# Optimization experiments

Measured on AMD Instinct MI355X. Metric: run time of the kernel, lower is better.

Reference implementation:

```python
import jax, jax.numpy as jnp
import numpy as np


def setup_inputs() -> dict:
    key = jax.random.key(0)
    ks = jax.random.split(key, 6)
    H = 1024
    NB = 5
    B = H  # required by the module's gate broadcasting (gate shape [B] * candidate [B,H])
    T = 128
    return {
        "features": jax.random.normal(ks[0], (B, T, H), dtype=jnp.float32),
        "states": jax.random.normal(ks[1], (NB * H,), dtype=jnp.float32),
        "Uw": jax.random.normal(ks[2], (H, H), dtype=jnp.float32) * 0.02,
        "Vw": jax.random.normal(ks[3], (H, H), dtype=jnp.float32) * 0.02,
        "Ww": jax.random.normal(ks[4], (H, H), dtype=jnp.float32) * 0.02,
        "keys": jax.random.normal(ks[5], (NB, H), dtype=jnp.float32) * 0.02,
        "prelu_a": jnp.ones((H,), dtype=jnp.float32),
    }


def reference(features, states, Uw, Vw, Ww, keys, prelu_a):
    # features: [B, T, H]; take CLS token (input_all_tokens=True)
    enc = features[:, 0, :]                      # [B, H]
    NB, H = keys.shape
    h = states.reshape(NB, H)                    # chunked states, [NB, H]

    # gate_i = sigmoid(enc @ h_i + enc @ key_i), vectorized over blocks -> [B, NB]
    gate = jax.nn.sigmoid(enc @ (h + keys).T)

    # candidate_i = PReLU(U(h_i) + V(key_i) + W(enc)) -> [NB, B, H]
    pre = (h @ Uw.T + keys @ Vw.T)[:, None, :] + (enc @ Ww.T)[None, :, :]
    cand = jnp.where(pre >= 0, pre, prelu_a * pre)

    # torch broadcasting of gate [B] against [B, H] aligns trailing dims (B == H),
    # so gate indexes the FEATURE axis: new[i, b, j] = h[i, j] + gate[j, i] * cand[i, b, j]
    new = h[:, None, :] + gate.T[:, None, :] * cand  # [NB, B, H]

    # in-place zero replacement aliases hidden_i in the original, so zeros -> 0.1 -> 1 after normalize
    new = jnp.where(new == 0, jnp.asarray(0.1, new.dtype), new)
    new = new / jnp.abs(new)

    # torch.cat(new_states) along dim 0 -> [NB*B, H]
    return new.reshape(NB * new.shape[1], H)
```

## Files before the change

kernel.cpp:

```cpp
#include <hip/hip_runtime.h>

#define H 1024
#define NB 5
#define TSTRIDE 131072

#define BM 64
#define BN 64
#define BK 32
#define LDA 68

__device__ __forceinline__ float sign_val(float h, float g, float pre, float a) {
    float cand = (pre >= 0.0f) ? pre : a * pre;
    float v = h + g * cand;
    if (v == 0.0f) v = 0.1f;
    return (v > 0.0f) ? 1.0f : -1.0f;
}

__global__ __launch_bounds__(256) void prep_kernel(
    const float* __restrict__ features,
    const float* __restrict__ states,
    const float* __restrict__ Uw,
    const float* __restrict__ Vw,
    const float* __restrict__ keys,
    float* __restrict__ gateT,
    float* __restrict__ baseT)
{
    const int j = blockIdx.x;
    const int tid = threadIdx.x;
    float accg[NB] = {0.f, 0.f, 0.f, 0.f, 0.f};
    float accb[NB] = {0.f, 0.f, 0.f, 0.f, 0.f};
    const float* encRow = features + (size_t)j * TSTRIDE;
    const float* uRow = Uw + (size_t)j * H;
    const float* vRow = Vw + (size_t)j * H;
    for (int k = tid; k < H; k += 256) {
        const float e = encRow[k];
        const float u = uRow[k];
        const float v = vRow[k];
        #pragma unroll
        for (int n = 0; n < NB; ++n) {
            const float hk = states[n * H + k];
            const float ky = keys[n * H + k];
            accg[n] += e * (hk + ky);
            accb[n] += hk * u + ky * v;
        }
    }
    __shared__ float red[2 * NB][4];
    #pragma unroll
    for (int n = 0; n < NB; ++n) {
        float g = accg[n], b = accb[n];
        #pragma unroll
        for (int off = 32; off > 0; off >>= 1) {
            g += __shfl_down(g, (unsigned)off, 64);
            b += __shfl_down(b, (unsigned)off, 64);
        }
        if ((tid & 63) == 0) {
            red[n][tid >> 6] = g;
            red[NB + n][tid >> 6] = b;
        }
    }
    __syncthreads();
    if (tid < 2 * NB) {
        const float s = red[tid][0] + red[tid][1] + red[tid][2] + red[tid][3];
        if (tid < NB) {
            gateT[tid * H + j] = 1.0f / (1.0f + expf(-s));
        } else {
            baseT[(tid - NB) * H + j] = s;
        }
    }
}

__global__ __launch_bounds__(256) void gemm_sign_kernel(
    const float* __restrict__ features,
    const float* __restrict__ Ww,
    const float* __restrict__ states,
    const float* __restrict__ prelu_a,
    const float* __restrict__ gateT,
    const float* __restrict__ baseT,
    float* __restrict__ out)
{
    __shared__ float As[BK][LDA];
    __shared__ float Bs[BK][LDA];
    const int bb = blockIdx.y * BM;
    const int jb = blockIdx.x * BN;
    const int tid = (int)threadIdx.x;
    const int tx = tid & 15;
    const int ty = tid >> 4;

    float acc[4][4] = {};

    for (int k0 = 0; k0 < H; k0 += BK) {
        #pragma unroll
        for (int l = 0; l < 2; ++l) {
            const int f = tid + l * 256;
            const int row = f >> 3;
            const int kq = (f & 7) << 2;
            const float4 av = *(const float4*)(features + (size_t)(bb + row) * TSTRIDE + k0 + kq);
            const float4 bv = *(const float4*)(Ww + (size_t)(jb + row) * H + k0 + kq);
            As[kq + 0][row] = av.x; As[kq + 1][row] = av.y;
            As[kq + 2][row] = av.z; As[kq + 3][row] = av.w;
            Bs[kq + 0][row] = bv.x; Bs[kq + 1][row] = bv.y;
            Bs[kq + 2][row] = bv.z; Bs[kq + 3][row] = bv.w;
        }
        __syncthreads();
        #pragma unroll
        for (int kk = 0; kk < BK; ++kk) {
            const float4 a = *(const float4*)&As[kk][ty << 2];
            const float4 b = *(const float4*)&Bs[kk][tx << 2];
            acc[0][0] += a.x * b.x; acc[0][1] += a.x * b.y; acc[0][2] += a.x * b.z; acc[0][3] += a.x * b.w;
            acc[1][0] += a.y * b.x; acc[1][1] += a.y * b.y; acc[1][2] += a.y * b.z; acc[1][3] += a.y * b.w;
            acc[2][0] += a.z * b.x; acc[2][1] += a.z * b.y; acc[2][2] += a.z * b.z; acc[2][3] += a.z * b.w;
            acc[3][0] += a.w * b.x; acc[3][1] += a.w * b.y; acc[3][2] += a.w * b.z; acc[3][3] += a.w * b.w;
        }
        __syncthreads();
    }

    const int c = jb + (tx << 2);
    const float4 pa = *(const float4*)(prelu_a + c);
    #pragma unroll
    for (int n = 0; n < NB; ++n) {
        const float4 hv = *(const float4*)(states + n * H + c);
        const float4 gv = *(const float4*)(gateT + n * H + c);
        const float4 sv = *(const float4*)(baseT + n * H + c);
        #pragma unroll
        for (int i = 0; i < 4; ++i) {
            float4 o;
            o.x = sign_val(hv.x, gv.x, sv.x + acc[i][0], pa.x);
            o.y = sign_val(hv.y, gv.y, sv.y + acc[i][1], pa.y);
            o.z = sign_val(hv.z, gv.z, sv.z + acc[i][2], pa.z);
            o.w = sign_val(hv.w, gv.w, sv.w + acc[i][3], pa.w);
            const int row = bb + (ty << 2) + i;
            *(float4*)(out + ((size_t)(n * H + row) * H + c)) = o;
        }
    }
}

extern "C" void kernel_launch(void* const* d_in, const int* in_sizes, int n_in,
                              void* d_out, int out_size, void* d_ws, size_t ws_size,
                              hipStream_t stream) {
    const float* features = (const float*)d_in[0];
    const float* states   = (const float*)d_in[1];
    const float* Uw       = (const float*)d_in[2];
    const float* Vw       = (const float*)d_in[3];
    const float* Ww       = (const float*)d_in[4];
    const float* keys     = (const float*)d_in[5];
    const float* prelu_a  = (const float*)d_in[6];
    float* out = (float*)d_out;

    float* gateT = (float*)d_ws;
    float* baseT = gateT + NB * H;

    prep_kernel<<<H, 256, 0, stream>>>(features, states, Uw, Vw, keys, gateT, baseT);

    dim3 grid(H / BN, H / BM);
    gemm_sign_kernel<<<grid, 256, 0, stream>>>(features, Ww, states, prelu_a,
                                               gateT, baseT, out);
}
```

Before: 640.9 us.

## Compact CLS rows in prep kernel and prefetch next GEMM tile into registers

The prep kernel now writes the CLS-token rows of features into a dense workspace buffer. The GEMM reads that buffer instead of the strided features tensor, so A-tile loads stop skipping through memory at a 512 KB row stride. The GEMM main loop also issues the global loads for the next K tile into registers while computing on the current shared-memory tile. This hides load latency at the cost of extra registers and an extra 4 MB write/read through the workspace.

```diff
diff --git a/kernel.cpp b/kernel.cpp
--- a/kernel.cpp
+++ b/kernel.cpp
@@ -23,7 +23,8 @@
     const float* __restrict__ Vw,
     const float* __restrict__ keys,
     float* __restrict__ gateT,
-    float* __restrict__ baseT)
+    float* __restrict__ baseT,
+    float* __restrict__ enc_c)
 {
     const int j = blockIdx.x;
     const int tid = threadIdx.x;
@@ -36,6 +37,7 @@
         const float e = encRow[k];
         const float u = uRow[k];
         const float v = vRow[k];
+        enc_c[(size_t)j * H + k] = e;
         #pragma unroll
         for (int n = 0; n < NB; ++n) {
             const float hk = states[n * H + k];
@@ -70,7 +72,7 @@
 }
 
 __global__ __launch_bounds__(256) void gemm_sign_kernel(
-    const float* __restrict__ features,
+    const float* __restrict__ enc_c,
     const float* __restrict__ Ww,
     const float* __restrict__ states,
     const float* __restrict__ prelu_a,
@@ -86,22 +88,39 @@
     const int tx = tid & 15;
     const int ty = tid >> 4;
 
+    const int f0 = tid,        row0 = f0 >> 3, kq0 = (f0 & 7) << 2;
+    const int f1 = tid + 256,  row1 = f1 >> 3, kq1 = (f1 & 7) << 2;
+    const float* aP0 = enc_c + (size_t)(bb + row0) * H + kq0;
+    const float* aP1 = enc_c + (size_t)(bb + row1) * H + kq1;
+    const float* bP0 = Ww    + (size_t)(jb + row0) * H + kq0;
+    const float* bP1 = Ww    + (size_t)(jb + row1) * H + kq1;
+
     float acc[4][4] = {};
 
-    for (int k0 = 0; k0 < H; k0 += BK) {
-        #pragma unroll
-        for (int l = 0; l < 2; ++l) {
-            const int f = tid + l * 256;
-            const int row = f >> 3;
-            const int kq = (f & 7) << 2;
-            const float4 av = *(const float4*)(features + (size_t)(bb + row) * TSTRIDE + k0 + kq);
-            const float4 bv = *(const float4*)(Ww + (size_t)(jb + row) * H + k0 + kq);
-            As[kq + 0][row] = av.x; As[kq + 1][row] = av.y;
-            As[kq + 2][row] = av.z; As[kq + 3][row] = av.w;
-            Bs[kq + 0][row] = bv.x; Bs[kq + 1][row] = bv.y;
-            Bs[kq + 2][row] = bv.z; Bs[kq + 3][row] = bv.w;
-        }
+    float4 a0 = *(const float4*)(aP0);
+    float4 a1 = *(const float4*)(aP1);
+    float4 b0 = *(const float4*)(bP0);
+    float4 b1 = *(const float4*)(bP1);
+
+    const int NK0 = H / BK;
+    for (int it = 0; it < NK0; ++it) {
         __syncthreads();
+        As[kq0 + 0][row0] = a0.x; As[kq0 + 1][row0] = a0.y;
+        As[kq0 + 2][row0] = a0.z; As[kq0 + 3][row0] = a0.w;
+        As[kq1 + 0][row1] = a1.x; As[kq1 + 1][row1] = a1.y;
+        As[kq1 + 2][row1] = a1.z; As[kq1 + 3][row1] = a1.w;
+        Bs[kq0 + 0][row0] = b0.x; Bs[kq0 + 1][row0] = b0.y;
+        Bs[kq0 + 2][row0] = b0.z; Bs[kq0 + 3][row0] = b0.w;
+        Bs[kq1 + 0][row1] = b1.x; Bs[kq1 + 1][row1] = b1.y;
+        Bs[kq1 + 2][row1] = b1.z; Bs[kq1 + 3][row1] = b1.w;
+        __syncthreads();
+
+        const int knext = (it + 1 < NK0) ? (it + 1) * BK : 0;
+        a0 = *(const float4*)(aP0 + knext);
+        a1 = *(const float4*)(aP1 + knext);
+        b0 = *(const float4*)(bP0 + knext);
+        b1 = *(const float4*)(bP1 + knext);
+
         #pragma unroll
         for (int kk = 0; kk < BK; ++kk) {
             const float4 a = *(const float4*)&As[kk][ty << 2];
@@ -111,7 +130,6 @@
             acc[2][0] += a.z * b.x; acc[2][1] += a.z * b.y; acc[2][2] += a.z * b.z; acc[2][3] += a.z * b.w;
             acc[3][0] += a.w * b.x; acc[3][1] += a.w * b.y; acc[3][2] += a.w * b.z; acc[3][3] += a.w * b.w;
         }
-        __syncthreads();
     }
 
     const int c = jb + (tx << 2);
@@ -148,10 +166,12 @@
 
     float* gateT = (float*)d_ws;
     float* baseT = gateT + NB * H;
+    float* enc_c = baseT + NB * H;
 
-    prep_kernel<<<H, 256, 0, stream>>>(features, states, Uw, Vw, keys, gateT, baseT);
+    prep_kernel<<<H, 256, 0, stream>>>(features, states, Uw, Vw, keys,
+                                       gateT, baseT, enc_c);
 
     dim3 grid(H / BN, H / BM);
-    gemm_sign_kernel<<<grid, 256, 0, stream>>>(features, Ww, states, prelu_a,
+    gemm_sign_kernel<<<grid, 256, 0, stream>>>(enc_c, Ww, states, prelu_a,
                                                gateT, baseT, out);
 }
```

After: 642.9 us. Within noise of the previous version (+0.3%).
